# Kernel optimization log

Measured on AMD Instinct MI355X. Metric: run time of the kernel, lower is better.

## Reference

```python
import jax, jax.numpy as jnp
import numpy as np

VIEWS = 16
TEMP = 0.07
BASE_TEMP = 0.07
EPS = 1e-12


def setup_inputs() -> dict:
    key = jax.random.key(0)
    k1, k2 = jax.random.split(key)
    features = jax.random.normal(k1, (8192, 128), dtype=jnp.float32)  # [bsz*views, d]
    labels = jax.random.randint(k2, (512,), 0, 100, dtype=jnp.int64 if jax.config.jax_enable_x64 else jnp.int32)
    return {"features": features, "labels": labels}


def reference(features, labels):
    bsz = labels.shape[0]                 # 512
    d = features.shape[-1]                # 128
    f = features.reshape(bsz, VIEWS, d)
    # F.normalize(p=2, dim=-1) with eps clamp
    norm = jnp.maximum(jnp.linalg.norm(f, axis=-1, keepdims=True), EPS)
    f = f / norm

    # positive mask from labels: [bsz, bsz]
    mask = (labels[:, None] == labels[None, :]).astype(jnp.float32)

    # contrast_feature = cat(unbind(f, dim=1)) -> view-major ordering
    contrast = jnp.transpose(f, (1, 0, 2)).reshape(VIEWS * bsz, d)  # [N, d]
    N = VIEWS * bsz

    # similarity logits, row-max stabilized (max is detached in torch)
    logits = jnp.matmul(contrast, contrast.T) / TEMP                 # [N, N]
    logits = logits - jax.lax.stop_gradient(jnp.max(logits, axis=1, keepdims=True))

    big_mask = jnp.tile(mask, (VIEWS, VIEWS))                        # [N, N]
    logits_mask = 1.0 - jnp.eye(N, dtype=jnp.float32)                # zero self-contrast
    big_mask = big_mask * logits_mask

    exp_logits = jnp.exp(logits) * logits_mask
    log_prob = logits - jnp.log(jnp.sum(exp_logits, axis=1, keepdims=True) + EPS)
    mean_log_prob_pos = jnp.sum(big_mask * log_prob, axis=1) / (jnp.sum(big_mask, axis=1) + EPS)

    loss = -(TEMP / BASE_TEMP) * mean_log_prob_pos                   # [N]
    return jnp.mean(loss.reshape(VIEWS, bsz))
```

## Files before the change

kernel.cpp:

```cpp
#include <hip/hip_runtime.h>
#include <hip/hip_bf16.h>

#define VIEWS 16
#define BSZ 512
#define NROWS 8192
#define D 128
#define CSPLIT 16
#define BCOLS 64
#define NSVC 100

typedef short bf16x8 __attribute__((ext_vector_type(8)));
typedef float f32x4 __attribute__((ext_vector_type(4)));

constexpr float C1 = 20.609929155556618f;
constexpr float INV_T = 14.285714285714286f;

__device__ __forceinline__ float bf2f(unsigned int u16) {
  return __uint_as_float(u16 << 16);
}

__device__ __forceinline__ unsigned short f2bf(float f) {
  unsigned int u = __float_as_uint(f);
  u += 0x7fffu + ((u >> 16) & 1u);
  return (unsigned short)(u >> 16);
}

__device__ __forceinline__ float fexp2(float x) {
#if __has_builtin(__builtin_amdgcn_exp2f)
  return __builtin_amdgcn_exp2f(x);
#else
  return exp2f(x);
#endif
}

__global__ __launch_bounds__(512) void k_norm_t(const float* __restrict__ feat,
                                                unsigned short* __restrict__ nrm,
                                                float* __restrict__ diag,
                                                float* __restrict__ T,
                                                float* __restrict__ out) {
  __shared__ float ldsT[VIEWS][D];
  int b = blockIdx.x;
  int t = threadIdx.x;
  if (b == 0 && t == 0) out[0] = 0.f;
  int v = t >> 5;
  int d0 = (t & 31) * 4;
  const float* src = feat + (size_t)(b * VIEWS + v) * D + d0;
  float4 x = *(const float4*)src;
  float ss = x.x * x.x + x.y * x.y + x.z * x.z + x.w * x.w;
#pragma unroll
  for (int m = 1; m < 32; m <<= 1) ss += __shfl_xor(ss, m);
  float inv = 1.0f / fmaxf(sqrtf(ss), 1e-12f);
  unsigned int u0 = f2bf(x.x * inv), u1 = f2bf(x.y * inv);
  unsigned int u2 = f2bf(x.z * inv), u3 = f2bf(x.w * inv);
  int n = v * BSZ + b;
  uint2 packed = {u0 | (u1 << 16), u2 | (u3 << 16)};
  *(uint2*)(nrm + (size_t)n * D + d0) = packed;
  float a0 = bf2f(u0), a1 = bf2f(u1), a2 = bf2f(u2), a3 = bf2f(u3);
  float ds = a0 * a0 + a1 * a1 + a2 * a2 + a3 * a3;
#pragma unroll
  for (int m = 1; m < 32; m <<= 1) ds += __shfl_xor(ds, m);
  if ((t & 31) == 0) diag[n] = ds;
  ldsT[v][d0] = a0;
  ldsT[v][d0 + 1] = a1;
  ldsT[v][d0 + 2] = a2;
  ldsT[v][d0 + 3] = a3;
  __syncthreads();
  if (t < D) {
    float acc = 0.f;
#pragma unroll
    for (int vv = 0; vv < VIEWS; ++vv) acc += ldsT[vv][t];
    T[(size_t)b * D + t] = acc;
  }
}

__global__ __launch_bounds__(512, 4) void k_gram_fused(
    const short* __restrict__ nrm, float* __restrict__ epart,
    const float* __restrict__ T, const int* __restrict__ labels,
    float* __restrict__ sv, int* __restrict__ cntc) {
  __shared__ __align__(16) char lds_raw[2][BCOLS][256];
  int tid = threadIdx.x;

  if (blockIdx.x < NSVC) {
    int* lab = (int*)&lds_raw[0][0][0];
    float* part = (float*)(&lds_raw[0][0][0] + 2048);
    int* pcnt = (int*)(&lds_raw[0][0][0] + 4096);
    int c = blockIdx.x;
    int q = tid >> 7;
    int d = tid & 127;
    lab[tid] = labels[tid];
    __syncthreads();
    float acc = 0.f;
    int count = 0;
#pragma unroll 4
    for (int b = q * 128; b < q * 128 + 128; ++b) {
      bool m = (lab[b] == c);
      float tv = T[(size_t)b * D + d];
      acc += m ? tv : 0.f;
      count += m ? 1 : 0;
    }
    part[q * D + d] = acc;
    if (d == 0) pcnt[q] = count;
    __syncthreads();
    if (tid < D) {
      sv[c * D + tid] = part[tid] + part[D + tid] + part[2 * D + tid] + part[3 * D + tid];
      if (tid == 0) cntc[c] = pcnt[0] + pcnt[1] + pcnt[2] + pcnt[3];
    }
    return;
  }

  int bid = blockIdx.x - NSVC;
  int rowblk = bid & 31;
  int cchunk = bid >> 5;
  int wid = tid >> 6;
  int lane = tid & 63;
  int idx = lane & 15;
  int kg = lane >> 4;
  int rowbase = rowblk * 256 + wid * 32;

  int srow = tid >> 4;
  int soff = (tid & 15) * 16;
  int swoff = srow * 256 + (soff ^ ((srow & 7) << 4));
  const char* gsrc = (const char*)nrm + (size_t)(cchunk * (NROWS / CSPLIT) + srow) * 256 + soff;

  bf16x8 afrag[2][4];
#pragma unroll
  for (int s = 0; s < 2; ++s)
#pragma unroll
    for (int c = 0; c < 4; ++c)
      afrag[s][c] = *(const bf16x8*)(nrm + (size_t)(rowbase + s * 16 + idx) * D + c * 32 + kg * 8);

  {
    uint4 v0 = *(const uint4*)gsrc;
    uint4 v1 = *(const uint4*)(gsrc + 32 * 256);
    *(uint4*)(&lds_raw[0][0][0] + swoff) = v0;
    *(uint4*)(&lds_raw[0][0][0] + swoff + 32 * 256) = v1;
  }

  f32x4 eloc[2][4];
#pragma unroll
  for (int s = 0; s < 2; ++s)
#pragma unroll
    for (int g = 0; g < 4; ++g)
#pragma unroll
      for (int r = 0; r < 4; ++r) eloc[s][g][r] = 0.f;

  __syncthreads();

  const int NT = (NROWS / CSPLIT) / BCOLS;
  const int rdsw = (idx & 7) << 4;
#pragma unroll 1
  for (int t = 0; t < NT; ++t) {
    uint4 s0, s1;
    if (t + 1 < NT) {
      const char* gp = gsrc + (size_t)(t + 1) * (BCOLS * 256);
      s0 = *(const uint4*)gp;
      s1 = *(const uint4*)(gp + 32 * 256);
    }

    const char* buf = &lds_raw[t & 1][0][0];
#pragma unroll
    for (int g = 0; g < 4; ++g) {
      bf16x8 bfrag[4];
#pragma unroll
      for (int c = 0; c < 4; ++c)
        bfrag[c] = *(const bf16x8*)(buf + (g * 16 + idx) * 256 + ((c * 64 + kg * 16) ^ rdsw));
#pragma unroll
      for (int s = 0; s < 2; ++s) {
        f32x4 acc = {0.f, 0.f, 0.f, 0.f};
#pragma unroll
        for (int c = 0; c < 4; ++c)
          acc = __builtin_amdgcn_mfma_f32_16x16x32_bf16(afrag[s][c], bfrag[c], acc, 0, 0, 0);
#pragma unroll
        for (int r = 0; r < 4; ++r)
          eloc[s][g][r] += fexp2(acc[r] * C1 - C1);
      }
    }

    if (t + 1 < NT) {
      char* wb = &lds_raw[(t + 1) & 1][0][0];
      *(uint4*)(wb + swoff) = s0;
      *(uint4*)(wb + swoff + 32 * 256) = s1;
    }
    __syncthreads();
  }

#pragma unroll
  for (int s = 0; s < 2; ++s)
#pragma unroll
    for (int r = 0; r < 4; ++r) {
      float vv = eloc[s][0][r] + eloc[s][1][r] + eloc[s][2][r] + eloc[s][3][r];
      vv += __shfl_xor(vv, 1);
      vv += __shfl_xor(vv, 2);
      vv += __shfl_xor(vv, 4);
      vv += __shfl_xor(vv, 8);
      if (idx == 0)
        epart[(size_t)cchunk * NROWS + rowbase + s * 16 + kg * 4 + r] = vv;
    }
}

__global__ __launch_bounds__(256) void k_final(const unsigned int* __restrict__ nrm_u32,
                                               const float* __restrict__ diag,
                                               const float* __restrict__ epart,
                                               const float* __restrict__ sv,
                                               const int* __restrict__ labels,
                                               const int* __restrict__ cntc,
                                               float* __restrict__ out) {
  int w = threadIdx.x >> 6;
  int lane = threadIdx.x & 63;
  int wg = blockIdx.x * 4 + w;
  float lsum = 0.f;
#pragma unroll 1
  for (int i = 0; i < 16; ++i) {
    int n = wg * 16 + i;
    int b = n & (BSZ - 1);
    int lbl = labels[b];
    float2 s2 = *(const float2*)(sv + lbl * D + lane * 2);
    unsigned int u = nrm_u32[(size_t)n * (D / 2) + lane];
    float a0 = bf2f(u & 0xffffu), a1 = bf2f(u >> 16);
    float dot = a0 * s2.x + a1 * s2.y;
    float ep = (lane < CSPLIT) ? epart[(size_t)lane * NROWS + n] : 0.f;
#pragma unroll
    for (int m = 1; m < 64; m <<= 1) {
      dot += __shfl_xor(dot, m);
      ep += __shfl_xor(ep, m);
    }
    if (lane == 0) {
      float dii = diag[n];
      float Praw = dot - dii;
      float Cn = (float)(16 * cntc[lbl] - 1);
      float ediag = fexp2(dii * C1 - C1);
      float Eexcl = ep - ediag;
      float Sref = Eexcl * fexp2((1.0f - dii) * C1);
      float L = logf(Sref + 1e-12f);
      float mlpp = (Praw * INV_T - Cn * (dii * INV_T) - Cn * L) / (Cn + 1e-12f);
      lsum += -mlpp;
    }
  }
  __shared__ float part[4];
  if (lane == 0) part[w] = lsum;
  __syncthreads();
  if (threadIdx.x == 0)
    atomicAdd(out, (part[0] + part[1] + part[2] + part[3]) * (1.0f / NROWS));
}

extern "C" void kernel_launch(void* const* d_in, const int* in_sizes, int n_in,
                              void* d_out, int out_size, void* d_ws, size_t ws_size,
                              hipStream_t stream) {
  const float* feat = (const float*)d_in[0];
  const int* labels = (const int*)d_in[1];
  float* out = (float*)d_out;
  char* ws = (char*)d_ws;

  size_t off = 0;
  short* nrm = (short*)(ws + off);           off += (size_t)NROWS * D * 2;
  float* diag = (float*)(ws + off);          off += (size_t)NROWS * 4;
  float* epart = (float*)(ws + off);         off += (size_t)NROWS * CSPLIT * 4;
  float* sv = (float*)(ws + off);            off += (size_t)128 * D * 4;
  int* cntc = (int*)(ws + off);              off += (size_t)128 * 4;
  float* T = (float*)(ws + off);             off += (size_t)BSZ * D * 4;

  k_norm_t<<<BSZ, 512, 0, stream>>>(feat, (unsigned short*)nrm, diag, T, out);
  k_gram_fused<<<NSVC + 32 * CSPLIT, 512, 0, stream>>>(nrm, epart, T, labels, sv, cntc);
  k_final<<<128, 256, 0, stream>>>((const unsigned int*)nrm, diag, epart, sv, labels, cntc, out);
}
```

Before: 47.99 us.

## Fuse final loss reduction into gram kernel via last-block atomic counters

Removes the separate k_final launch. Each gram row-block increments a per-rowblock counter, and the last of the CSPLIT column chunks to finish computes the loss terms for its 256 rows. It first spin-waits until all 100 class-sum blocks have signalled completion. This saves a kernel launch and its dependency gap, at the cost of fences, atomics, a spin-wait that relies on those blocks being scheduled, and fewer blocks (32) doing the final pass.

```diff
diff --git a/kernel.cpp b/kernel.cpp
--- a/kernel.cpp
+++ b/kernel.cpp
@@ -37,11 +37,15 @@
                                                 unsigned short* __restrict__ nrm,
                                                 float* __restrict__ diag,
                                                 float* __restrict__ T,
-                                                float* __restrict__ out) {
+                                                float* __restrict__ out,
+                                                int* __restrict__ cnt) {
   __shared__ float ldsT[VIEWS][D];
   int b = blockIdx.x;
   int t = threadIdx.x;
-  if (b == 0 && t == 0) out[0] = 0.f;
+  if (b == 0) {
+    if (t == 0) out[0] = 0.f;
+    if (t < 33) cnt[t] = 0;
+  }
   int v = t >> 5;
   int d0 = (t & 31) * 4;
   const float* src = feat + (size_t)(b * VIEWS + v) * D + d0;
@@ -76,7 +80,9 @@
 __global__ __launch_bounds__(512, 4) void k_gram_fused(
     const short* __restrict__ nrm, float* __restrict__ epart,
     const float* __restrict__ T, const int* __restrict__ labels,
-    float* __restrict__ sv, int* __restrict__ cntc) {
+    float* __restrict__ sv, int* __restrict__ cntc,
+    const float* __restrict__ diag, float* __restrict__ out,
+    int* __restrict__ cnt) {
   __shared__ __align__(16) char lds_raw[2][BCOLS][256];
   int tid = threadIdx.x;
 
@@ -105,6 +111,9 @@
       sv[c * D + tid] = part[tid] + part[D + tid] + part[2 * D + tid] + part[3 * D + tid];
       if (tid == 0) cntc[c] = pcnt[0] + pcnt[1] + pcnt[2] + pcnt[3];
     }
+    __threadfence();
+    __syncthreads();
+    if (tid == 0) atomicAdd(&cnt[32], 1);
     return;
   }
 
@@ -196,22 +205,28 @@
       if (idx == 0)
         epart[(size_t)cchunk * NROWS + rowbase + s * 16 + kg * 4 + r] = vv;
     }
-}
-
-__global__ __launch_bounds__(256) void k_final(const unsigned int* __restrict__ nrm_u32,
-                                               const float* __restrict__ diag,
-                                               const float* __restrict__ epart,
-                                               const float* __restrict__ sv,
-                                               const int* __restrict__ labels,
-                                               const int* __restrict__ cntc,
-                                               float* __restrict__ out) {
-  int w = threadIdx.x >> 6;
-  int lane = threadIdx.x & 63;
-  int wg = blockIdx.x * 4 + w;
+
+  __threadfence();
+  __syncthreads();
+  __shared__ int is_last;
+  if (tid == 0) {
+    int old = atomicAdd(&cnt[rowblk], 1);
+    is_last = (old == CSPLIT - 1) ? 1 : 0;
+  }
+  __syncthreads();
+  if (!is_last) return;
+
+  if (tid == 0) {
+    while (atomicAdd(&cnt[32], 0) < NSVC) { }
+  }
+  __syncthreads();
+  __threadfence();
+
+  const unsigned int* nrm_u32 = (const unsigned int*)nrm;
   float lsum = 0.f;
 #pragma unroll 1
-  for (int i = 0; i < 16; ++i) {
-    int n = wg * 16 + i;
+  for (int i = 0; i < 32; ++i) {
+    int n = rowblk * 256 + wid * 32 + i;
     int b = n & (BSZ - 1);
     int lbl = labels[b];
     float2 s2 = *(const float2*)(sv + lbl * D + lane * 2);
@@ -236,11 +251,14 @@
       lsum += -mlpp;
     }
   }
-  __shared__ float part[4];
-  if (lane == 0) part[w] = lsum;
-  __syncthreads();
-  if (threadIdx.x == 0)
-    atomicAdd(out, (part[0] + part[1] + part[2] + part[3]) * (1.0f / NROWS));
+  __shared__ float fpart[8];
+  if (lane == 0) fpart[wid] = lsum;
+  __syncthreads();
+  if (tid == 0) {
+    float s = fpart[0] + fpart[1] + fpart[2] + fpart[3] +
+              fpart[4] + fpart[5] + fpart[6] + fpart[7];
+    atomicAdd(out, s * (1.0f / NROWS));
+  }
 }
 
 extern "C" void kernel_launch(void* const* d_in, const int* in_sizes, int n_in,
@@ -258,8 +276,9 @@
   float* sv = (float*)(ws + off);            off += (size_t)128 * D * 4;
   int* cntc = (int*)(ws + off);              off += (size_t)128 * 4;
   float* T = (float*)(ws + off);             off += (size_t)BSZ * D * 4;
-
-  k_norm_t<<<BSZ, 512, 0, stream>>>(feat, (unsigned short*)nrm, diag, T, out);
-  k_gram_fused<<<NSVC + 32 * CSPLIT, 512, 0, stream>>>(nrm, epart, T, labels, sv, cntc);
-  k_final<<<128, 256, 0, stream>>>((const unsigned int*)nrm, diag, epart, sv, labels, cntc, out);
-}
+  int* cnt = (int*)(ws + off);               off += (size_t)128 * 4;
+
+  k_norm_t<<<BSZ, 512, 0, stream>>>(feat, (unsigned short*)nrm, diag, T, out, cnt);
+  k_gram_fused<<<NSVC + 32 * CSPLIT, 512, 0, stream>>>(nrm, epart, T, labels, sv, cntc,
+                                                       diag, out, cnt);
+}
```

After: 155.0 us. 223% more time.
